# Kernel tuning notes

Hardware: AMD Instinct MI355X
Metric: run time of the kernel (lower is better)

Reference implementation:

```python
import jax, jax.numpy as jnp
import numpy as np

B, C, D, H = 2, 1024, 1024, 16
DH = D // H
EPS = 1e-8


def setup_inputs() -> dict:
    key = jax.random.key(0)
    ks = jax.random.split(key, 12)
    s = 0.02
    return {
        "x": jax.random.normal(ks[0], (B, C, D), dtype=jnp.float32),
        "rms_w": jnp.ones((C, D), dtype=jnp.float32),
        "rms_b": jnp.zeros((C, D), dtype=jnp.float32),
        "Wqkv": jax.random.normal(ks[1], (3 * D, D), dtype=jnp.float32) * s,
        "Wout": jax.random.normal(ks[2], (D, D), dtype=jnp.float32) * s,
        "bout": jnp.zeros((D,), dtype=jnp.float32),
        "Wf": jax.random.normal(ks[3], (D, D), dtype=jnp.float32) * s,
        "bf": jnp.zeros((D,), dtype=jnp.float32),
        "Ww": jax.random.normal(ks[4], (D, D), dtype=jnp.float32) * s,
        "bw": jnp.zeros((D,), dtype=jnp.float32),
        "Wv": jax.random.normal(ks[5], (D, D), dtype=jnp.float32) * s,
        "bv": jnp.zeros((D,), dtype=jnp.float32),
        "beta": jnp.ones((1,), dtype=jnp.float32),
    }


def _rope_cos_sin(C, dh):
    # faithful to source: theta = 10000 ** (-2*(i-1)/dh), i in [0, dh//2)
    i = jnp.arange(dh // 2, dtype=jnp.float32)
    theta = 10000.0 ** (-2.0 * (i - 1.0) / dh)            # [dh//2]
    ang = jnp.arange(C, dtype=jnp.float32)[:, None] * theta  # [C, dh//2]
    return jnp.cos(ang), jnp.sin(ang)


def _rotate(t, cos, sin):
    # equivalent to einsum('bhci,cij->bhcj', t, R) with the source R
    ev, od = t[..., 0::2], t[..., 1::2]          # [B,H,C,dh//2]
    out_ev = ev * cos + od * sin
    out_od = -ev * sin + od * cos
    return jnp.stack([out_ev, out_od], axis=-1).reshape(t.shape)


def _rmsnorm(x, w, b):
    rms = jnp.sqrt(jnp.mean(x * x, axis=-1, keepdims=True) + EPS)
    return w * (x / rms) + b


def _attention(x, Wqkv, Wout, bout):
    qkv = x @ Wqkv.T                               # [B,C,3D]
    q, k, v = jnp.split(qkv, 3, axis=-1)
    def heads(t):
        return t.reshape(B, C, H, DH).transpose(0, 2, 1, 3)  # [B,H,C,dh]
    q, k, v = heads(q), heads(k), heads(v)
    cos, sin = _rope_cos_sin(C, DH)
    qr = _rotate(q, cos, sin)
    kr = _rotate(k, cos, sin)
    scale = 1.0 / jnp.sqrt(jnp.float32(DH))
    num = jnp.exp(jnp.einsum('bhid,bhjd->bhij', qr, kr) * scale)
    den = jnp.sum(jnp.exp(jnp.einsum('bhid,bhjd->bhij', q, k) * scale),
                  axis=-1, keepdims=True)
    attn = num / den
    mask = jnp.tril(jnp.ones((C, C), dtype=bool))
    attn = jnp.where(mask[None, None], attn, 0.0)
    y = attn @ v                                   # [B,H,C,dh]
    y = y.transpose(0, 2, 1, 3).reshape(B, C, D)
    return y @ Wout.T + bout


def _ffn(x, Wf, bf, Ww, bw, Wv, bv, beta):
    h = x @ Wf.T + bf
    wx = h @ Ww.T + bw
    swish = wx * jax.nn.sigmoid(beta * wx)
    return swish * (h @ Wv.T + bv)


def reference(x, rms_w, rms_b, Wqkv, Wout, bout, Wf, bf, Ww, bw, Wv, bv, beta):
    # dropout p is identity in eval mode
    x = _rmsnorm(x, rms_w, rms_b)
    x = x + _attention(x, Wqkv, Wout, bout)
    x = _rmsnorm(x, rms_w, rms_b)   # same shared RMSNorm module applied twice
    x = x + _ffn(x, Wf, bf, Ww, bw, Wv, bv, beta)
    return x
```

## Files before the change

### kernel.cpp

```cpp
#include <hip/hip_runtime.h>
#include <math.h>

#define B_ 2
#define C_ 1024
#define D_ 1024
#define H_ 16
#define DH_ 64
#define EPSF 1e-8f
#define BK 64

typedef __bf16 bf16;
typedef __attribute__((ext_vector_type(4))) __bf16 bf16x4;
typedef __attribute__((ext_vector_type(8))) __bf16 bf16x8;
typedef __attribute__((ext_vector_type(4))) float f32x4;

__device__ inline f32x4 mfma16(bf16x8 a, bf16x8 b, f32x4 c) {
  return __builtin_amdgcn_mfma_f32_16x16x32_bf16(a, b, c, 0, 0, 0);
}

__device__ inline void async16(const bf16* g, bf16* l) {
  __builtin_amdgcn_global_load_lds((const __attribute__((address_space(1))) void*)g,
                                   (__attribute__((address_space(3))) void*)l, 16, 0, 0);
}

__device__ inline float rope_theta(float i) {
  return exp2f(-13.287712379549449f * (2.0f * (i - 1.0f) * (1.0f / 64.0f)));
}

__global__ __launch_bounds__(256) void cvt_rms_kernel(const float* __restrict__ wqkv,
                                                      const float* __restrict__ wout,
                                                      const float* __restrict__ wf,
                                                      const float* __restrict__ www,
                                                      const float* __restrict__ wv,
                                                      bf16* __restrict__ wdst,
                                                      const float* __restrict__ x,
                                                      const float* __restrict__ rw,
                                                      const float* __restrict__ rb,
                                                      bf16* __restrict__ xout) {
  __shared__ float red[4];
  int t = threadIdx.x;
  if (blockIdx.x < 7 * 1024) {
    int seg = blockIdx.x >> 10;
    int local = (blockIdx.x & 1023) * 1024 + t * 4;
    const float* src = seg < 3 ? wqkv + (size_t)seg * (D_ * D_)
                     : seg == 3 ? wout : seg == 4 ? wf : seg == 5 ? www : wv;
    float4 v = *(const float4*)(src + local);
    bf16x4 o;
    o[0] = (bf16)v.x; o[1] = (bf16)v.y; o[2] = (bf16)v.z; o[3] = (bf16)v.w;
    *(bf16x4*)(wdst + (size_t)seg * (D_ * D_) + local) = o;
    return;
  }
  int row = blockIdx.x - 7 * 1024;
  int c = row & (C_ - 1);
  float4 xv = *(const float4*)(x + (size_t)row * D_ + t * 4);
  float ss = xv.x * xv.x + xv.y * xv.y + xv.z * xv.z + xv.w * xv.w;
#pragma unroll
  for (int m = 1; m < 64; m <<= 1) ss += __shfl_xor(ss, m, 64);
  if ((t & 63) == 0) red[t >> 6] = ss;
  __syncthreads();
  float tot = red[0] + red[1] + red[2] + red[3];
  float inv = rsqrtf(tot * (1.0f / D_) + EPSF);
  float4 wv4 = *(const float4*)(rw + (size_t)c * D_ + t * 4);
  float4 bv4 = *(const float4*)(rb + (size_t)c * D_ + t * 4);
  bf16x4 ov;
  ov[0] = (bf16)(wv4.x * (xv.x * inv) + bv4.x);
  ov[1] = (bf16)(wv4.y * (xv.y * inv) + bv4.y);
  ov[2] = (bf16)(wv4.z * (xv.z * inv) + bv4.z);
  ov[3] = (bf16)(wv4.w * (xv.w * inv) + bv4.w);
  *(bf16x4*)(xout + (size_t)row * D_ + t * 4) = ov;
}

__global__ __launch_bounds__(256) void rmsnorm_bf16_kernel(const bf16* __restrict__ x,
                                                           const float* __restrict__ w,
                                                           const float* __restrict__ b,
                                                           bf16* __restrict__ out) {
  int row = blockIdx.x;
  int c = row & (C_ - 1);
  int t = threadIdx.x;
  bf16x4 xv = *(const bf16x4*)(x + (size_t)row * D_ + t * 4);
  float f0 = (float)xv[0], f1 = (float)xv[1], f2 = (float)xv[2], f3 = (float)xv[3];
  float ss = f0 * f0 + f1 * f1 + f2 * f2 + f3 * f3;
#pragma unroll
  for (int m = 1; m < 64; m <<= 1) ss += __shfl_xor(ss, m, 64);
  __shared__ float red[4];
  if ((t & 63) == 0) red[t >> 6] = ss;
  __syncthreads();
  float tot = red[0] + red[1] + red[2] + red[3];
  float inv = rsqrtf(tot * (1.0f / D_) + EPSF);
  float4 wv = *(const float4*)(w + (size_t)c * D_ + t * 4);
  float4 bv = *(const float4*)(b + (size_t)c * D_ + t * 4);
  bf16x4 ov;
  ov[0] = (bf16)(wv.x * (f0 * inv) + bv.x);
  ov[1] = (bf16)(wv.y * (f1 * inv) + bv.y);
  ov[2] = (bf16)(wv.z * (f2 * inv) + bv.z);
  ov[3] = (bf16)(wv.w * (f3 * inv) + bv.w);
  *(bf16x4*)(out + (size_t)row * D_ + t * 4) = ov;
}

template <int BMt, int BNt>
__global__ __launch_bounds__(256) void gemm_lds(const bf16* __restrict__ A,
                                                const bf16* __restrict__ W,
                                                const float* __restrict__ bias,
                                                const bf16* __restrict__ R,
                                                bf16* __restrict__ Cout,
                                                int M, int N, int K) {
  constexpr int MT = BMt / 32;
  constexpr int NT = BNt / 32;
  __shared__ bf16 sa[BMt * BK];
  __shared__ bf16 sb[BNt * BK];
  int t = threadIdx.x, l = t & 63, w = t >> 6;
  int m0 = blockIdx.y * BMt;
  int n0 = blockIdx.x * BNt;
  int wm = (w >> 1) * (BMt / 2), wn = (w & 1) * (BNt / 2);
  int lm = l & 15, lq = l >> 4;
  int swz = lm & 7;
  f32x4 acc[MT][NT] = {};

  for (int k0 = 0; k0 < K; k0 += BK) {
    __syncthreads();
#pragma unroll
    for (int p = 0; p < BMt / 32; ++p) {
      int lin = p * 256 + t;
      int r = lin >> 3, cc = (lin & 7) ^ (r & 7);
      async16(A + (size_t)(m0 + r) * K + k0 + cc * 8, sa + lin * 8);
    }
#pragma unroll
    for (int p = 0; p < BNt / 32; ++p) {
      int lin = p * 256 + t;
      int r = lin >> 3, cc = (lin & 7) ^ (r & 7);
      async16(W + (size_t)(n0 + r) * K + k0 + cc * 8, sb + lin * 8);
    }
    __syncthreads();
    bf16x8 af[MT][2], bfr[NT][2];
#pragma unroll
    for (int mt = 0; mt < MT; ++mt) {
      const bf16* base = sa + (wm + mt * 16 + lm) * BK;
      af[mt][0] = *(const bf16x8*)(base + ((lq ^ swz) << 3));
      af[mt][1] = *(const bf16x8*)(base + (((4 | lq) ^ swz) << 3));
    }
#pragma unroll
    for (int nt = 0; nt < NT; ++nt) {
      const bf16* base = sb + (wn + nt * 16 + lm) * BK;
      bfr[nt][0] = *(const bf16x8*)(base + ((lq ^ swz) << 3));
      bfr[nt][1] = *(const bf16x8*)(base + (((4 | lq) ^ swz) << 3));
    }
#pragma unroll
    for (int mt = 0; mt < MT; ++mt)
#pragma unroll
      for (int nt = 0; nt < NT; ++nt) {
        acc[mt][nt] = mfma16(af[mt][0], bfr[nt][0], acc[mt][nt]);
        acc[mt][nt] = mfma16(af[mt][1], bfr[nt][1], acc[mt][nt]);
      }
  }
#pragma unroll
  for (int mt = 0; mt < MT; ++mt)
#pragma unroll
    for (int nt = 0; nt < NT; ++nt) {
      int col = n0 + wn + nt * 16 + lm;
      float bb = bias ? bias[col] : 0.0f;
#pragma unroll
      for (int r = 0; r < 4; ++r) {
        int row = m0 + wm + mt * 16 + lq * 4 + r;
        float v = acc[mt][nt][r] + bb;
        if (R) v += (float)R[(size_t)row * N + col];
        Cout[(size_t)row * N + col] = (bf16)v;
      }
    }
}

__global__ __launch_bounds__(256) void gemm_qkv_kernel(const bf16* __restrict__ A,
                                                       const bf16* __restrict__ W,
                                                       bf16* __restrict__ qkv,
                                                       bf16* __restrict__ kr,
                                                       bf16* __restrict__ vt) {
  constexpr int BMt = 128, BNt = 64, MT = 4, NT = 2;
  const int N = 3 * D_, K = D_;
  __shared__ bf16 sa[BMt * BK];
  __shared__ bf16 sb[BNt * BK];
  __shared__ bf16 tv[64 * 136];
  int t = threadIdx.x, l = t & 63, w = t >> 6;
  int m0 = blockIdx.y * BMt;
  int n0 = blockIdx.x * BNt;
  int wm = (w >> 1) * 64, wn = (w & 1) * 32;
  int lm = l & 15, lq = l >> 4;
  int swz = lm & 7;
  f32x4 acc[MT][NT] = {};

  for (int k0 = 0; k0 < K; k0 += BK) {
    __syncthreads();
#pragma unroll
    for (int p = 0; p < 4; ++p) {
      int lin = p * 256 + t;
      int r = lin >> 3, cc = (lin & 7) ^ (r & 7);
      async16(A + (size_t)(m0 + r) * K + k0 + cc * 8, sa + lin * 8);
    }
#pragma unroll
    for (int p = 0; p < 2; ++p) {
      int lin = p * 256 + t;
      int r = lin >> 3, cc = (lin & 7) ^ (r & 7);
      async16(W + (size_t)(n0 + r) * K + k0 + cc * 8, sb + lin * 8);
    }
    __syncthreads();
    bf16x8 af[MT][2], bfr[NT][2];
#pragma unroll
    for (int mt = 0; mt < MT; ++mt) {
      const bf16* base = sa + (wm + mt * 16 + lm) * BK;
      af[mt][0] = *(const bf16x8*)(base + ((lq ^ swz) << 3));
      af[mt][1] = *(const bf16x8*)(base + (((4 | lq) ^ swz) << 3));
    }
#pragma unroll
    for (int nt = 0; nt < NT; ++nt) {
      const bf16* base = sb + (wn + nt * 16 + lm) * BK;
      bfr[nt][0] = *(const bf16x8*)(base + ((lq ^ swz) << 3));
      bfr[nt][1] = *(const bf16x8*)(base + (((4 | lq) ^ swz) << 3));
    }
#pragma unroll
    for (int mt = 0; mt < MT; ++mt)
#pragma unroll
      for (int nt = 0; nt < NT; ++nt) {
        acc[mt][nt] = mfma16(af[mt][0], bfr[nt][0], acc[mt][nt]);
        acc[mt][nt] = mfma16(af[mt][1], bfr[nt][1], acc[mt][nt]);
      }
  }
  if (n0 < 2 * D_) {
    bool isK = n0 >= D_;
#pragma unroll
    for (int mt = 0; mt < MT; ++mt)
#pragma unroll
      for (int nt = 0; nt < NT; ++nt) {
        int col = n0 + wn + nt * 16 + lm;
        float th = isK ? rope_theta((float)(((col - D_) & 63) >> 1)) : 0.0f;
#pragma unroll
        for (int r = 0; r < 4; ++r) {
          int row = m0 + wm + mt * 16 + lq * 4 + r;
          float v = acc[mt][nt][r];
          qkv[(size_t)row * N + col] = (bf16)v;
          if (isK) {
            float other = __shfl_xor(v, 1, 64);
            float ang = (float)(row & (C_ - 1)) * th;
            float s_, c_;
            __sincosf(ang, &s_, &c_);
            float rot = (col & 1) ? (v * c_ - other * s_)
                                  : (v * c_ + other * s_);
            kr[(size_t)row * D_ + (col - D_)] = (bf16)rot;
          }
        }
      }
  } else {
#pragma unroll
    for (int mt = 0; mt < MT; ++mt)
#pragma unroll
      for (int nt = 0; nt < NT; ++nt) {
        int dh = wn + nt * 16 + lm;
#pragma unroll
        for (int r = 0; r < 4; ++r)
          tv[dh * 136 + wm + mt * 16 + lq * 4 + r] = (bf16)acc[mt][nt][r];
      }
    __syncthreads();
    int h = (n0 - 2 * D_) >> 6;
    int bb = m0 >> 10;
    int mloc = m0 & 1023;
    size_t vbase = (size_t)((bb * H_ + h) * DH_) * C_;
#pragma unroll
    for (int p = 0; p < 4; ++p) {
      int lin = p * 256 + t;
      int dh = lin >> 4;
      int mm = (lin & 15) * 8;
      *(int4*)(vt + vbase + (size_t)dh * C_ + mloc + mm) = *(int4*)(tv + dh * 136 + mm);
    }
  }
}

__global__ __launch_bounds__(256) void gemm_ffn_kernel(const bf16* __restrict__ A,
                                                       const bf16* __restrict__ Ww,
                                                       const bf16* __restrict__ Wv,
                                                       const float* __restrict__ bw,
                                                       const float* __restrict__ bv,
                                                       const bf16* __restrict__ x3,
                                                       const float* __restrict__ beta_p,
                                                       float* __restrict__ out) {
  __shared__ bf16 sa[64 * BK];
  __shared__ bf16 sb1[64 * BK];
  __shared__ bf16 sb2[64 * BK];
  int t = threadIdx.x, l = t & 63, w = t >> 6;
  int m0 = blockIdx.y * 64, n0 = blockIdx.x * 64;
  int wm = (w >> 1) * 32, wn = (w & 1) * 32;
  int lm = l & 15, lq = l >> 4;
  int swz = lm & 7;
  float beta = beta_p[0];
  f32x4 acc1[2][2] = {}, acc2[2][2] = {};

  for (int k0 = 0; k0 < D_; k0 += BK) {
    __syncthreads();
#pragma unroll
    for (int p = 0; p < 2; ++p) {
      int lin = p * 256 + t;
      int r = lin >> 3, cc = (lin & 7) ^ (r & 7);
      async16(A + (size_t)(m0 + r) * D_ + k0 + cc * 8, sa + lin * 8);
      async16(Ww + (size_t)(n0 + r) * D_ + k0 + cc * 8, sb1 + lin * 8);
      async16(Wv + (size_t)(n0 + r) * D_ + k0 + cc * 8, sb2 + lin * 8);
    }
    __syncthreads();
    bf16x8 af[2][2], b1f[2][2], b2f[2][2];
#pragma unroll
    for (int mt = 0; mt < 2; ++mt) {
      const bf16* base = sa + (wm + mt * 16 + lm) * BK;
      af[mt][0] = *(const bf16x8*)(base + ((lq ^ swz) << 3));
      af[mt][1] = *(const bf16x8*)(base + (((4 | lq) ^ swz) << 3));
    }
#pragma unroll
    for (int nt = 0; nt < 2; ++nt) {
      const bf16* base1 = sb1 + (wn + nt * 16 + lm) * BK;
      const bf16* base2 = sb2 + (wn + nt * 16 + lm) * BK;
      b1f[nt][0] = *(const bf16x8*)(base1 + ((lq ^ swz) << 3));
      b1f[nt][1] = *(const bf16x8*)(base1 + (((4 | lq) ^ swz) << 3));
      b2f[nt][0] = *(const bf16x8*)(base2 + ((lq ^ swz) << 3));
      b2f[nt][1] = *(const bf16x8*)(base2 + (((4 | lq) ^ swz) << 3));
    }
#pragma unroll
    for (int mt = 0; mt < 2; ++mt)
#pragma unroll
      for (int nt = 0; nt < 2; ++nt) {
        acc1[mt][nt] = mfma16(af[mt][0], b1f[nt][0], acc1[mt][nt]);
        acc1[mt][nt] = mfma16(af[mt][1], b1f[nt][1], acc1[mt][nt]);
        acc2[mt][nt] = mfma16(af[mt][0], b2f[nt][0], acc2[mt][nt]);
        acc2[mt][nt] = mfma16(af[mt][1], b2f[nt][1], acc2[mt][nt]);
      }
  }
#pragma unroll
  for (int mt = 0; mt < 2; ++mt)
#pragma unroll
    for (int nt = 0; nt < 2; ++nt) {
      int col = n0 + wn + nt * 16 + lm;
      float bbw = bw[col], bbv = bv[col];
#pragma unroll
      for (int r = 0; r < 4; ++r) {
        int row = m0 + wm + mt * 16 + lq * 4 + r;
        float z = acc1[mt][nt][r] + bbw;
        float g = acc2[mt][nt][r] + bbv;
        float sw_ = z / (1.0f + __expf(-beta * z));
        out[(size_t)row * D_ + col] = (float)x3[(size_t)row * D_ + col] + sw_ * g;
      }
    }
}

__global__ __launch_bounds__(256) void attn_kernel(const bf16* __restrict__ qkv,
                                                   const bf16* __restrict__ kr,
                                                   const bf16* __restrict__ vt,
                                                   bf16* __restrict__ y) {
  __shared__ bf16 sk[64 * 72];
  __shared__ bf16 skr[64 * 72];
  __shared__ bf16 sv[64 * 72];
  __shared__ bf16 pl[4][16 * 72];
  int t = threadIdx.x, l = t & 63, w = t >> 6;
  int blk = blockIdx.x;
  int idx = blk & 255;
  int it = (blk < 256) ? (idx >> 5) : (15 - (idx >> 5));
  int r5 = idx & 31;
  int b = r5 >> 4;
  int h = r5 & 15;
  int i_base = it * 64 + w * 16;
  int lm = l & 15, lq = l >> 4;
  const float scale = 0.125f;

  size_t hq = (size_t)h * DH_;
  size_t qrow = (size_t)(b * C_ + i_base + lm) * (3 * D_) + hq;
  bf16x8 qp[2], qrf[2];
  float cq = (float)(i_base + lm);
#pragma unroll
  for (int kk = 0; kk < 2; ++kk) {
    qp[kk] = *(const bf16x8*)(qkv + qrow + kk * 32 + lq * 8);
#pragma unroll
    for (int j = 0; j < 4; ++j) {
      float ip = (float)(kk * 16 + lq * 4 + j);
      float ang = cq * rope_theta(ip);
      float sv_, cv_;
      __sincosf(ang, &sv_, &cv_);
      float qe = (float)qp[kk][2 * j], qo = (float)qp[kk][2 * j + 1];
      qrf[kk][2 * j] = (bf16)(qe * cv_ + qo * sv_);
      qrf[kk][2 * j + 1] = (bf16)(qo * cv_ - qe * sv_);
    }
  }

  float den[4] = {0.f, 0.f, 0.f, 0.f};
  f32x4 yacc[4] = {};
  int i_max = i_base + 15;
  size_t kbase = (size_t)(b * C_) * (3 * D_) + D_ + hq;
  size_t krbase = (size_t)(b * C_) * D_ + hq;
  size_t vtbase = (size_t)((b * H_ + h) * DH_) * C_;
  int sr = t >> 3;
  int sc = (t & 7) * 8;

  int4 pk0, pk1, pr0, pr1, pv0, pv1;
#define FETCH_TILE(J0)                                                          \
  pk0 = *(const int4*)(qkv + kbase + (size_t)((J0) + sr) * (3 * D_) + sc);      \
  pk1 = *(const int4*)(qkv + kbase + (size_t)((J0) + 32 + sr) * (3 * D_) + sc); \
  pr0 = *(const int4*)(kr + krbase + (size_t)((J0) + sr) * D_ + sc);            \
  pr1 = *(const int4*)(kr + krbase + (size_t)((J0) + 32 + sr) * D_ + sc);       \
  pv0 = *(const int4*)(vt + vtbase + (size_t)sr * C_ + (J0) + sc);              \
  pv1 = *(const int4*)(vt + vtbase + (size_t)(32 + sr) * C_ + (J0) + sc);

  FETCH_TILE(0)

  for (int j0 = 0; j0 < C_; j0 += 64) {
    __syncthreads();
    *(int4*)(sk + sr * 72 + sc) = pk0;
    *(int4*)(sk + (32 + sr) * 72 + sc) = pk1;
    *(int4*)(skr + sr * 72 + sc) = pr0;
    *(int4*)(skr + (32 + sr) * 72 + sc) = pr1;
    *(int4*)(sv + sr * 72 + sc) = pv0;
    *(int4*)(sv + (32 + sr) * 72 + sc) = pv1;
    __syncthreads();
    if (j0 + 64 < C_) {
      FETCH_TILE(j0 + 64)
    }
#pragma unroll
    for (int js = 0; js < 64; js += 16) {
      bf16x8 kf0 = *(const bf16x8*)(sk + (js + lm) * 72 + lq * 8);
      bf16x8 kf1 = *(const bf16x8*)(sk + (js + lm) * 72 + 32 + lq * 8);
      f32x4 s = {0.f, 0.f, 0.f, 0.f};
      s = mfma16(qp[0], kf0, s);
      s = mfma16(qp[1], kf1, s);
#pragma unroll
      for (int r = 0; r < 4; ++r) den[r] += __expf(s[r] * scale);
    }
    if (j0 <= i_max) {
#pragma unroll
      for (int js = 0; js < 64; js += 16) {
        bf16x8 kf0 = *(const bf16x8*)(skr + (js + lm) * 72 + lq * 8);
        bf16x8 kf1 = *(const bf16x8*)(skr + (js + lm) * 72 + 32 + lq * 8);
        f32x4 s = {0.f, 0.f, 0.f, 0.f};
        s = mfma16(qrf[0], kf0, s);
        s = mfma16(qrf[1], kf1, s);
#pragma unroll
        for (int r = 0; r < 4; ++r) {
          int jg = j0 + js + lm;
          int ig = i_base + lq * 4 + r;
          float p = (jg <= ig) ? __expf(s[r] * scale) : 0.0f;
          pl[w][(lq * 4 + r) * 72 + js + lm] = (bf16)p;
        }
      }
      __builtin_amdgcn_wave_barrier();
      bf16x8 pf0 = *(const bf16x8*)(pl[w] + lm * 72 + lq * 8);
      bf16x8 pf1 = *(const bf16x8*)(pl[w] + lm * 72 + 32 + lq * 8);
#pragma unroll
      for (int tt = 0; tt < 4; ++tt) {
        bf16x8 vf0 = *(const bf16x8*)(sv + (tt * 16 + lm) * 72 + lq * 8);
        bf16x8 vf1 = *(const bf16x8*)(sv + (tt * 16 + lm) * 72 + 32 + lq * 8);
        yacc[tt] = mfma16(pf0, vf0, mfma16(pf1, vf1, yacc[tt]));
      }
      __builtin_amdgcn_wave_barrier();
    }
  }
#undef FETCH_TILE
  float inv[4];
#pragma unroll
  for (int r = 0; r < 4; ++r) {
    float d = den[r];
    d += __shfl_xor(d, 1, 64);
    d += __shfl_xor(d, 2, 64);
    d += __shfl_xor(d, 4, 64);
    d += __shfl_xor(d, 8, 64);
    inv[r] = 1.0f / d;
  }
#pragma unroll
  for (int tt = 0; tt < 4; ++tt)
#pragma unroll
    for (int r = 0; r < 4; ++r) {
      int ig = i_base + lq * 4 + r;
      y[(size_t)(b * C_ + ig) * D_ + hq + tt * 16 + lm] = (bf16)(yacc[tt][r] * inv[r]);
    }
}

extern "C" void kernel_launch(void* const* d_in, const int* in_sizes, int n_in,
                              void* d_out, int out_size, void* d_ws, size_t ws_size,
                              hipStream_t stream) {
  const float* x = (const float*)d_in[0];
  const float* rms_w = (const float*)d_in[1];
  const float* rms_b = (const float*)d_in[2];
  const float* Wqkv = (const float*)d_in[3];
  const float* Wout = (const float*)d_in[4];
  const float* bout = (const float*)d_in[5];
  const float* Wf = (const float*)d_in[6];
  const float* bfp = (const float*)d_in[7];
  const float* Ww = (const float*)d_in[8];
  const float* bw = (const float*)d_in[9];
  const float* Wv = (const float*)d_in[10];
  const float* bv = (const float*)d_in[11];
  const float* beta = (const float*)d_in[12];
  float* out = (float*)d_out;

  bf16* ws = (bf16*)d_ws;
  const size_t DD = (size_t)D_ * D_;
  const size_t MC = (size_t)B_ * C_;
  bf16* wb = ws;
  bf16* x1 = ws + 7 * DD;
  bf16* qkv = ws + 9 * DD;
  bf16* vt = ws + 15 * DD;
  bf16* x2 = ws + 17 * DD;
  bf16* x3 = ws + 19 * DD;
  bf16* hbuf = ws + 21 * DD;
  bf16* krb = ws + 23 * DD;
  bf16* y = (bf16*)d_out;

  cvt_rms_kernel<<<7 * 1024 + MC, 256, 0, stream>>>(Wqkv, Wout, Wf, Ww, Wv, wb, x, rms_w,
                                                    rms_b, x1);
  gemm_qkv_kernel<<<dim3(3 * D_ / 64, MC / 128), 256, 0, stream>>>(x1, wb, qkv, krb, vt);
  attn_kernel<<<B_ * H_ * 16, 256, 0, stream>>>(qkv, krb, vt, y);
  gemm_lds<64, 64><<<dim3(D_ / 64, MC / 64), 256, 0, stream>>>(
      y, wb + 3 * DD, bout, x1, x2, MC, D_, D_);
  rmsnorm_bf16_kernel<<<MC, 256, 0, stream>>>(x2, rms_w, rms_b, x3);
  gemm_lds<64, 64><<<dim3(D_ / 64, MC / 64), 256, 0, stream>>>(
      x3, wb + 4 * DD, bfp, nullptr, hbuf, MC, D_, D_);
  gemm_ffn_kernel<<<dim3(D_ / 64, MC / 64), 256, 0, stream>>>(
      hbuf, wb + 5 * DD, wb + 6 * DD, bw, bv, x3, beta, out);
}
```

Measured before the change: 206.0 us.

## Widen attention key tile to 128 and skip fully masked causal segments

The attention kernel now stages 128 keys per iteration instead of 64. This halves the number of block-wide barriers and refill rounds, at the cost of more prefetch registers and about double the LDS. Inside the causal part, each wave computes only the 32-key segments that can be unmasked for its rows and skips the P·V MFMAs for the rest, zeroing any skipped P slots. The inner P·V loop now has a runtime trip count, which may limit unrolling, and the larger LDS footprint may reduce occupancy.

```diff
diff --git a/kernel.cpp b/kernel.cpp
--- a/kernel.cpp
+++ b/kernel.cpp
@@ -348,10 +348,10 @@
                                                    const bf16* __restrict__ kr,
                                                    const bf16* __restrict__ vt,
                                                    bf16* __restrict__ y) {
-  __shared__ bf16 sk[64 * 72];
-  __shared__ bf16 skr[64 * 72];
-  __shared__ bf16 sv[64 * 72];
-  __shared__ bf16 pl[4][16 * 72];
+  __shared__ bf16 sk[128 * 72];
+  __shared__ bf16 skr[128 * 72];
+  __shared__ bf16 sv[64 * 136];
+  __shared__ bf16 pl[4][16 * 136];
   int t = threadIdx.x, l = t & 63, w = t >> 6;
   int blk = blockIdx.x;
   int idx = blk & 255;
@@ -391,31 +391,43 @@
   int sr = t >> 3;
   int sc = (t & 7) * 8;
 
-  int4 pk0, pk1, pr0, pr1, pv0, pv1;
+  int4 pk0, pk1, pk2, pk3, pr0, pr1, pr2, pr3, pv0, pv1, pv2, pv3;
 #define FETCH_TILE(J0)                                                          \
   pk0 = *(const int4*)(qkv + kbase + (size_t)((J0) + sr) * (3 * D_) + sc);      \
   pk1 = *(const int4*)(qkv + kbase + (size_t)((J0) + 32 + sr) * (3 * D_) + sc); \
+  pk2 = *(const int4*)(qkv + kbase + (size_t)((J0) + 64 + sr) * (3 * D_) + sc); \
+  pk3 = *(const int4*)(qkv + kbase + (size_t)((J0) + 96 + sr) * (3 * D_) + sc); \
   pr0 = *(const int4*)(kr + krbase + (size_t)((J0) + sr) * D_ + sc);            \
   pr1 = *(const int4*)(kr + krbase + (size_t)((J0) + 32 + sr) * D_ + sc);       \
+  pr2 = *(const int4*)(kr + krbase + (size_t)((J0) + 64 + sr) * D_ + sc);       \
+  pr3 = *(const int4*)(kr + krbase + (size_t)((J0) + 96 + sr) * D_ + sc);       \
   pv0 = *(const int4*)(vt + vtbase + (size_t)sr * C_ + (J0) + sc);              \
-  pv1 = *(const int4*)(vt + vtbase + (size_t)(32 + sr) * C_ + (J0) + sc);
+  pv1 = *(const int4*)(vt + vtbase + (size_t)(32 + sr) * C_ + (J0) + sc);       \
+  pv2 = *(const int4*)(vt + vtbase + (size_t)sr * C_ + (J0) + 64 + sc);         \
+  pv3 = *(const int4*)(vt + vtbase + (size_t)(32 + sr) * C_ + (J0) + 64 + sc);
 
   FETCH_TILE(0)
 
-  for (int j0 = 0; j0 < C_; j0 += 64) {
-    __syncthreads();
-    *(int4*)(sk + sr * 72 + sc) = pk0;
-    *(int4*)(sk + (32 + sr) * 72 + sc) = pk1;
-    *(int4*)(skr + sr * 72 + sc) = pr0;
-    *(int4*)(skr + (32 + sr) * 72 + sc) = pr1;
-    *(int4*)(sv + sr * 72 + sc) = pv0;
-    *(int4*)(sv + (32 + sr) * 72 + sc) = pv1;
-    __syncthreads();
-    if (j0 + 64 < C_) {
-      FETCH_TILE(j0 + 64)
-    }
-#pragma unroll
-    for (int js = 0; js < 64; js += 16) {
+  for (int j0 = 0; j0 < C_; j0 += 128) {
+    __syncthreads();
+    *(int4*)(sk + (size_t)sr * 72 + sc) = pk0;
+    *(int4*)(sk + (size_t)(32 + sr) * 72 + sc) = pk1;
+    *(int4*)(sk + (size_t)(64 + sr) * 72 + sc) = pk2;
+    *(int4*)(sk + (size_t)(96 + sr) * 72 + sc) = pk3;
+    *(int4*)(skr + (size_t)sr * 72 + sc) = pr0;
+    *(int4*)(skr + (size_t)(32 + sr) * 72 + sc) = pr1;
+    *(int4*)(skr + (size_t)(64 + sr) * 72 + sc) = pr2;
+    *(int4*)(skr + (size_t)(96 + sr) * 72 + sc) = pr3;
+    *(int4*)(sv + (size_t)sr * 136 + sc) = pv0;
+    *(int4*)(sv + (size_t)(32 + sr) * 136 + sc) = pv1;
+    *(int4*)(sv + (size_t)sr * 136 + 64 + sc) = pv2;
+    *(int4*)(sv + (size_t)(32 + sr) * 136 + 64 + sc) = pv3;
+    __syncthreads();
+    if (j0 + 128 < C_) {
+      FETCH_TILE(j0 + 128)
+    }
+#pragma unroll
+    for (int js = 0; js < 128; js += 16) {
       bf16x8 kf0 = *(const bf16x8*)(sk + (js + lm) * 72 + lq * 8);
       bf16x8 kf1 = *(const bf16x8*)(sk + (js + lm) * 72 + 32 + lq * 8);
       f32x4 s = {0.f, 0.f, 0.f, 0.f};
@@ -425,29 +437,38 @@
       for (int r = 0; r < 4; ++r) den[r] += __expf(s[r] * scale);
     }
     if (j0 <= i_max) {
-#pragma unroll
-      for (int js = 0; js < 64; js += 16) {
-        bf16x8 kf0 = *(const bf16x8*)(skr + (js + lm) * 72 + lq * 8);
-        bf16x8 kf1 = *(const bf16x8*)(skr + (js + lm) * 72 + 32 + lq * 8);
-        f32x4 s = {0.f, 0.f, 0.f, 0.f};
-        s = mfma16(qrf[0], kf0, s);
-        s = mfma16(qrf[1], kf1, s);
-#pragma unroll
-        for (int r = 0; r < 4; ++r) {
-          int jg = j0 + js + lm;
-          int ig = i_base + lq * 4 + r;
-          float p = (jg <= ig) ? __expf(s[r] * scale) : 0.0f;
-          pl[w][(lq * 4 + r) * 72 + js + lm] = (bf16)p;
+      int rel = i_max - j0;
+      int nseg = (rel >> 5) + 1;
+      if (nseg > 4) nseg = 4;
+      int jslim = nseg << 5;
+      for (int js = 0; js < jslim; js += 16) {
+        if (j0 + js <= i_max) {
+          bf16x8 kf0 = *(const bf16x8*)(skr + (js + lm) * 72 + lq * 8);
+          bf16x8 kf1 = *(const bf16x8*)(skr + (js + lm) * 72 + 32 + lq * 8);
+          f32x4 s = {0.f, 0.f, 0.f, 0.f};
+          s = mfma16(qrf[0], kf0, s);
+          s = mfma16(qrf[1], kf1, s);
+#pragma unroll
+          for (int r = 0; r < 4; ++r) {
+            int jg = j0 + js + lm;
+            int ig = i_base + lq * 4 + r;
+            float p = (jg <= ig) ? __expf(s[r] * scale) : 0.0f;
+            pl[w][(lq * 4 + r) * 136 + js + lm] = (bf16)p;
+          }
+        } else {
+#pragma unroll
+          for (int r = 0; r < 4; ++r)
+            pl[w][(lq * 4 + r) * 136 + js + lm] = (bf16)0.0f;
         }
       }
       __builtin_amdgcn_wave_barrier();
-      bf16x8 pf0 = *(const bf16x8*)(pl[w] + lm * 72 + lq * 8);
-      bf16x8 pf1 = *(const bf16x8*)(pl[w] + lm * 72 + 32 + lq * 8);
 #pragma unroll
       for (int tt = 0; tt < 4; ++tt) {
-        bf16x8 vf0 = *(const bf16x8*)(sv + (tt * 16 + lm) * 72 + lq * 8);
-        bf16x8 vf1 = *(const bf16x8*)(sv + (tt * 16 + lm) * 72 + 32 + lq * 8);
-        yacc[tt] = mfma16(pf0, vf0, mfma16(pf1, vf1, yacc[tt]));
+        for (int seg = 0; seg < nseg; ++seg) {
+          bf16x8 pf = *(const bf16x8*)(pl[w] + lm * 136 + seg * 32 + lq * 8);
+          bf16x8 vf = *(const bf16x8*)(sv + (tt * 16 + lm) * 136 + seg * 32 + lq * 8);
+          yacc[tt] = mfma16(pf, vf, yacc[tt]);
+        }
       }
       __builtin_amdgcn_wave_barrier();
     }
```

Result: slower. 211.5 us (+2.7%).
